# Kernel optimization log

Hardware: AMD Instinct MI355X
Metric: run time of the kernel (lower is better)

The kernel has to match this reference:

```python
import jax, jax.numpy as jnp
import numpy as np

V, N, D, R, L, KS = 32000, 2048, 1024, 16, 4, 7
B, H = 2, 4 * 1024
GMIN, GMAX, ACAP = 0.85, 1.0, 1.0


def rmsnorm(x, w, eps=1e-6):
    return x * jax.lax.rsqrt(jnp.mean(x * x, axis=-1, keepdims=True) + eps) * w


def l2norm(x, eps=1e-8):
    return x / jnp.maximum(jnp.linalg.norm(x, axis=-1, keepdims=True), eps)


def mlp(x, w1, b1, w2, b2):
    return jax.nn.gelu(x @ w1 + b1) @ w2 + b2


def k1_block(h, nw, w1, b1, w2, b2):
    return h + mlp(rmsnorm(h, nw), w1, b1, w2, b2)


def causal_conv(h, kernel):
    # depthwise causal conv with shared 1D kernel; kernel[0] = current step
    n = h.shape[1]
    hp = jnp.pad(h, ((0, 0), (KS - 1, 0), (0, 0)))
    out = jnp.zeros_like(h)
    for k in range(KS):  # KS is small & static
        out = out + kernel[k] * hp[:, KS - 1 - k: KS - 1 - k + n, :]
    return out


def k2_layer(h, p):
    (u, v, dlog, alog, glog, kern, pw, pb, n1w, n2w, w1, b1, w2, b2) = p
    residual = h
    hn = rmsnorm(h, n1w)
    gate = jax.nn.sigmoid(glog)
    out = gate * causal_conv(hn, kern)
    # low-rank q/k
    q = l2norm(hn @ u)          # (B,N,R)
    k = l2norm(hn @ v)          # (B,N,R)
    gamma = GMIN + (GMAX - GMIN) * jax.nn.sigmoid(dlog)   # (R,)
    alpha = ACAP * jax.nn.sigmoid(alog)                   # (R,)
    qa = q * alpha
    pos = jnp.arange(h.shape[1])
    diff = jnp.maximum(pos[:, None] - pos[None, :], 0).astype(h.dtype)
    mask = (pos[:, None] >= pos[None, :]).astype(h.dtype)
    # per-rank causal decay matrix gamma_r^(i-j): (R,N,N)
    decay = jnp.exp(diff[None] * jnp.log(gamma)[:, None, None]) * mask[None]
    scores = jnp.einsum('bir,rij,bjr->bij', qa, decay, k)  # (B,N,N)
    out = out + jnp.einsum('bij,bjd->bid', scores, hn)
    out = out @ pw + pb
    h = residual + out
    h = h + mlp(rmsnorm(h, n2w), w1, b1, w2, b2)
    return h


def setup_inputs() -> dict:
    key = jax.random.key(0)
    ks = jax.random.split(key, 32)
    f32 = jnp.float32
    inp = {
        'tokens': jax.random.randint(ks[0], (B, N), 0, V),
        'emb_table': jax.random.normal(ks[1], (V, D), f32) * 0.02,
        'k1a_nw': jnp.ones((D,), f32),
        'k1a_w1': jax.random.normal(ks[2], (D, H), f32) * 0.02,
        'k1a_b1': jnp.zeros((H,), f32),
        'k1a_w2': jax.random.normal(ks[3], (H, D), f32) * 0.02,
        'k1a_b2': jnp.zeros((D,), f32),
        'k2_u': jax.random.normal(ks[4], (L, D, R), f32) * 0.05,
        'k2_v': jax.random.normal(ks[5], (L, D, R), f32) * 0.05,
        'k2_dlog': jax.random.normal(ks[6], (L, R), f32) * 0.5,
        'k2_alog': jnp.zeros((L, R), f32),
        'k2_glog': jnp.zeros((L,), f32),
        'k2_kern': jax.random.normal(ks[7], (L, KS), f32) * 0.1,
        'k2_pw': jax.random.normal(ks[8], (L, D, D), f32) * 0.02,
        'k2_pb': jnp.zeros((L, D), f32),
        'k2_n1w': jnp.ones((L, D), f32),
        'k2_n2w': jnp.ones((L, D), f32),
        'k2_w1': jax.random.normal(ks[9], (L, D, H), f32) * 0.02,
        'k2_b1': jnp.zeros((L, H), f32),
        'k2_w2': jax.random.normal(ks[10], (L, H, D), f32) * 0.02,
        'k2_b2': jnp.zeros((L, D), f32),
        'k1b_nw': jnp.ones((D,), f32),
        'k1b_w1': jax.random.normal(ks[11], (D, H), f32) * 0.02,
        'k1b_b1': jnp.zeros((H,), f32),
        'k1b_w2': jax.random.normal(ks[12], (H, D), f32) * 0.02,
        'k1b_b2': jnp.zeros((D,), f32),
        'k0_nw': jnp.ones((D,), f32),
        'head_w': jax.random.normal(ks[13], (D, V), f32) * 0.02,
        'head_b': jnp.zeros((V,), f32),
    }
    return inp


def reference(tokens, emb_table,
              k1a_nw, k1a_w1, k1a_b1, k1a_w2, k1a_b2,
              k2_u, k2_v, k2_dlog, k2_alog, k2_glog, k2_kern,
              k2_pw, k2_pb, k2_n1w, k2_n2w, k2_w1, k2_b1, k2_w2, k2_b2,
              k1b_nw, k1b_w1, k1b_b1, k1b_w2, k1b_b2,
              k0_nw, head_w, head_b):
    h = emb_table[tokens]                                  # (B,N,D)
    h = k1_block(h, k1a_nw, k1a_w1, k1a_b1, k1a_w2, k1a_b2)
    stacked = (k2_u, k2_v, k2_dlog, k2_alog, k2_glog, k2_kern,
               k2_pw, k2_pb, k2_n1w, k2_n2w, k2_w1, k2_b1, k2_w2, k2_b2)
    def step(c, p):
        return k2_layer(c, p), None
    h, _ = jax.lax.scan(step, h, stacked)
    h = k1_block(h, k1b_nw, k1b_w1, k1b_b1, k1b_w2, k1b_b2)
    h = rmsnorm(h, k0_nw)                                  # K0 final norm
    return h @ head_w + head_b                             # (B,N,V)
```

## Files before the change

kernel.cpp:

```cpp
#include <hip/hip_runtime.h>
#include <hip/hip_bf16.h>

#define SEQ 2048
#define DIM 1024
#define RNK 16
#define NL 4
#define KT 7
#define BATCH 2
#define HID 4096
#define VOC 32000
#define BNROWS (BATCH*SEQ)
#define CHK 128
#define NCH (SEQ/CHK)
#define PRMS 128
#define KAPP 160

typedef __hip_bfloat16 bf16;
typedef __attribute__((ext_vector_type(8))) short bh8;
typedef __attribute__((ext_vector_type(4))) float vf4;

__device__ __forceinline__ float bfu(unsigned int u) { u <<= 16; return __builtin_bit_cast(float, u); }
__device__ __forceinline__ unsigned short f2bu(float x) { bf16 t = __float2bfloat16(x); return __builtin_bit_cast(unsigned short, t); }
__device__ __forceinline__ float b2f(bf16 x) { return __bfloat162float(x); }
__device__ __forceinline__ float sigm(float x) { return 1.f / (1.f + expf(-x)); }
__device__ __forceinline__ float gelu_t(float x) {
    float u = 0.7978845608028654f * (x + 0.044715f * x * x * x);
    return 0.5f * x * (1.f + tanhf(u));
}

__device__ __forceinline__ void gld16(const bf16* g, bf16* l) {
    __builtin_amdgcn_global_load_lds(
        (const __attribute__((address_space(1))) void*)g,
        (__attribute__((address_space(3))) void*)l,
        16, 0, 0);
}

__global__ void embed_kernel(const int* __restrict__ tokens, const float* __restrict__ emb,
                             float* __restrict__ h) {
    int row = blockIdx.x;
    int tok = tokens[row];
    const float4* src = (const float4*)(emb + (size_t)tok * DIM);
    float4* dst = (float4*)(h + (size_t)row * DIM);
    dst[threadIdx.x] = src[threadIdx.x];
}

__global__ void rmsnorm_kernel(const float* __restrict__ in, const float* __restrict__ wt,
                               bf16* __restrict__ out) {
    int row = blockIdx.x;
    int tx = threadIdx.x;
    float4 v = ((const float4*)(in + (size_t)row * DIM))[tx];
    float ss = v.x * v.x + v.y * v.y + v.z * v.z + v.w * v.w;
#pragma unroll
    for (int off = 32; off > 0; off >>= 1) ss += __shfl_down(ss, off);
    __shared__ float red[4];
    int lane = tx & 63, wv = tx >> 6;
    if (lane == 0) red[wv] = ss;
    __syncthreads();
    float tot = red[0] + red[1] + red[2] + red[3];
    float scale = rsqrtf(tot * (1.f / DIM) + 1e-6f);
    float4 w4 = ((const float4*)wt)[tx];
    uint2 o;
    o.x = f2bu(v.x * scale * w4.x) | ((unsigned int)f2bu(v.y * scale * w4.y) << 16);
    o.y = f2bu(v.z * scale * w4.z) | ((unsigned int)f2bu(v.w * scale * w4.w) << 16);
    *(uint2*)(out + (size_t)row * DIM + tx * 4) = o;
}

__global__ void transpose_cast_kernel(const float* __restrict__ in, bf16* __restrict__ out,
                                      int K, int Nc) {
    __shared__ float tile[32][33];
    int n0 = blockIdx.x * 32, k0 = blockIdx.y * 32;
    int tx = threadIdx.x & 31, ty = threadIdx.x >> 5;
#pragma unroll
    for (int i = 0; i < 32; i += 8)
        tile[ty + i][tx] = in[(size_t)(k0 + ty + i) * Nc + n0 + tx];
    __syncthreads();
#pragma unroll
    for (int i = 0; i < 32; i += 8)
        out[(size_t)(n0 + ty + i) * K + k0 + tx] = __float2bfloat16(tile[tx][ty + i]);
}

__global__ void prep_kernel(const float* __restrict__ dlog, const float* __restrict__ alog,
                            const float* __restrict__ glog, const float* __restrict__ kern,
                            float* __restrict__ prm) {
    int l = blockIdx.x, t = threadIdx.x;
    float* p = prm + l * PRMS;
    if (t < RNK) {
        float g = 0.85f + 0.15f * sigm(dlog[l * RNK + t]);
        float lg = logf(g);
        p[t] = g;
        p[16 + t] = lg;
        p[32 + t] = expf(lg * (float)CHK);
        p[48 + t] = sigm(alog[l * RNK + t]);
    }
    if (t < KT) {
        float gate = sigm(glog[l]);
        p[64 + t] = gate * kern[l * KT + t];
    }
}

__global__ void prep_uv_kernel(const float* __restrict__ u, const float* __restrict__ v,
                               bf16* __restrict__ uvT) {
    int l = blockIdx.y;
    int k = blockIdx.x * 256 + threadIdx.x;
    const float* ul = u + (size_t)l * DIM * RNK;
    const float* vl = v + (size_t)l * DIM * RNK;
    bf16* o = uvT + (size_t)l * 32 * DIM;
#pragma unroll
    for (int r = 0; r < RNK; ++r) {
        o[(size_t)r * DIM + k] = __float2bfloat16(ul[(size_t)k * RNK + r]);
        o[(size_t)(RNK + r) * DIM + k] = __float2bfloat16(vl[(size_t)k * RNK + r]);
    }
}

__global__ void conv_kernel(const bf16* __restrict__ hn, const float* __restrict__ prm,
                            float* __restrict__ Z) {
    int t = blockIdx.x * 256 + threadIdx.x;
    int d4 = (t & 255) * 4;
    int row = t >> 8;
    int n = row & (SEQ - 1);
    float a0 = 0, a1 = 0, a2 = 0, a3 = 0;
#pragma unroll
    for (int kk = 0; kk < KT; ++kk) {
        if (n - kk < 0) break;
        float wv = prm[64 + kk];
        uint2 hv = *(const uint2*)(hn + (size_t)(row - kk) * DIM + d4);
        a0 += wv * bfu(hv.x & 0xffffu);
        a1 += wv * bfu(hv.x >> 16);
        a2 += wv * bfu(hv.y & 0xffffu);
        a3 += wv * bfu(hv.y >> 16);
    }
    float4 o = {a0, a1, a2, a3};
    *(float4*)(Z + (size_t)row * DIM + d4) = o;
}

__global__ __launch_bounds__(64)
void qk_mfma_kernel(const bf16* __restrict__ hn, const bf16* __restrict__ uvT,
                    const float* __restrict__ prm, float* __restrict__ qa,
                    float* __restrict__ kn) {
    int row0 = blockIdx.x * 32;
    int lane = threadIdx.x;
    int fr = lane & 15, kf = (lane >> 4) * 8;
    vf4 acc[2][2] = {};
#pragma unroll 4
    for (int kt = 0; kt < DIM / 32; ++kt) {
        int k0 = kt * 32;
        bh8 b0 = *(const bh8*)(uvT + (size_t)fr * DIM + k0 + kf);
        bh8 b1 = *(const bh8*)(uvT + (size_t)(16 + fr) * DIM + k0 + kf);
        bh8 a0 = *(const bh8*)(hn + (size_t)(row0 + fr) * DIM + k0 + kf);
        bh8 a1 = *(const bh8*)(hn + (size_t)(row0 + 16 + fr) * DIM + k0 + kf);
        acc[0][0] = __builtin_amdgcn_mfma_f32_16x16x32_bf16(a0, b0, acc[0][0], 0, 0, 0);
        acc[0][1] = __builtin_amdgcn_mfma_f32_16x16x32_bf16(a0, b1, acc[0][1], 0, 0, 0);
        acc[1][0] = __builtin_amdgcn_mfma_f32_16x16x32_bf16(a1, b0, acc[1][0], 0, 0, 0);
        acc[1][1] = __builtin_amdgcn_mfma_f32_16x16x32_bf16(a1, b1, acc[1][1], 0, 0, 0);
    }
    int fq = lane >> 4;
    float alpha = prm[48 + fr];
#pragma unroll
    for (int m = 0; m < 2; ++m) {
#pragma unroll
        for (int j = 0; j < 4; ++j) {
            float qv = acc[m][0][j], kv = acc[m][1][j];
            float sq = qv * qv, sk = kv * kv;
#pragma unroll
            for (int mask = 1; mask < 16; mask <<= 1) {
                sq += __shfl_xor(sq, mask);
                sk += __shfl_xor(sk, mask);
            }
            int row = row0 + m * 16 + fq * 4 + j;
            qa[(size_t)row * RNK + fr] = qv / fmaxf(sqrtf(sq), 1e-8f) * alpha;
            kn[(size_t)row * RNK + fr] = kv / fmaxf(sqrtf(sk), 1e-8f);
        }
    }
}

__global__ void trans_hn_kernel(const bf16* __restrict__ hn, bf16* __restrict__ HB) {
    __shared__ bf16 tile[32][40];
    int bc = blockIdx.x;
    int d0 = blockIdx.y * 32, j0 = blockIdx.z * 32;
    int tx = threadIdx.x & 31, ty = threadIdx.x >> 5;
    size_t rowb = (size_t)bc * CHK;
#pragma unroll
    for (int i = 0; i < 32; i += 8)
        tile[ty + i][tx] = hn[(rowb + j0 + ty + i) * DIM + d0 + tx];
    __syncthreads();
    bf16* Hp = HB + (size_t)bc * DIM * KAPP;
#pragma unroll
    for (int i = 0; i < 32; i += 8)
        Hp[(size_t)(d0 + ty + i) * KAPP + j0 + tx] = tile[tx][ty + i];
}

__global__ void scores_kernel(const float* __restrict__ qa, const float* __restrict__ kn,
                              const float* __restrict__ prm, bf16* __restrict__ SA,
                              bf16* __restrict__ kdtB) {
    int bc = blockIdx.x;
    __shared__ float ptab[CHK][16];
    for (int e = threadIdx.x; e < CHK * 16; e += 256) {
        int tt = e >> 4, r = e & 15;
        ptab[tt][r] = expf(prm[16 + r] * (float)tt);
    }
    __syncthreads();
    size_t rowb = (size_t)bc * CHK;
    bf16* SAp = SA + (size_t)bc * CHK * KAPP;
    for (int e = threadIdx.x; e < CHK * CHK; e += 256) {
        int i = e >> 7, j = e & (CHK - 1);
        float vsum = 0.f;
        if (i >= j) {
            const float* qp = qa + (rowb + i) * RNK;
            const float* kp = kn + (rowb + j) * RNK;
#pragma unroll
            for (int r = 0; r < 16; ++r) vsum += qp[r] * ptab[i - j][r] * kp[r];
        }
        SAp[(size_t)i * KAPP + j] = __float2bfloat16(vsum);
    }
    for (int e = threadIdx.x; e < CHK * 32; e += 256) {
        int i = e >> 5, rr = e & 31;
        float w = 0.f;
        if (rr < 16) w = qa[(rowb + i) * RNK + rr] * expf(prm[16 + rr] * (float)(i + 1));
        SAp[(size_t)i * KAPP + CHK + rr] = __float2bfloat16(w);
    }
    bf16* kp2 = kdtB + (size_t)bc * RNK * CHK;
    for (int e = threadIdx.x; e < RNK * CHK; e += 256) {
        int r = e >> 7, j = e & (CHK - 1);
        kp2[e] = __float2bfloat16(ptab[CHK - 1 - j][r] * kn[(rowb + j) * RNK + r]);
    }
}

__global__ __launch_bounds__(64)
void chunkU_kernel(const bf16* __restrict__ HB, const bf16* __restrict__ kdtB,
                   float* __restrict__ U) {
    int bc = blockIdx.x;
    int d0 = blockIdx.y * 64;
    int lane = threadIdx.x;
    int fr = lane & 15, kf = (lane >> 4) * 8;
    const bf16* Hp = HB + (size_t)bc * DIM * KAPP;
    const bf16* Kp = kdtB + (size_t)bc * RNK * CHK;
    vf4 acc[4] = {};
#pragma unroll
    for (int kt = 0; kt < 4; ++kt) {
        int k0 = kt * 32;
        bh8 bb = *(const bh8*)(Kp + (size_t)fr * CHK + k0 + kf);
#pragma unroll
        for (int m = 0; m < 4; ++m) {
            bh8 a = *(const bh8*)(Hp + (size_t)(d0 + m * 16 + fr) * KAPP + k0 + kf);
            acc[m] = __builtin_amdgcn_mfma_f32_16x16x32_bf16(a, bb, acc[m], 0, 0, 0);
        }
    }
    int fq = lane >> 4;
    float* Up = U + (size_t)bc * DIM * RNK;
#pragma unroll
    for (int m = 0; m < 4; ++m)
#pragma unroll
        for (int j = 0; j < 4; ++j)
            Up[(size_t)(d0 + m * 16 + fq * 4 + j) * RNK + fr] = acc[m][j];
}

__global__ void scanP_kernel(const float* __restrict__ U, const float* __restrict__ prm,
                             bf16* __restrict__ HB) {
    int g = blockIdx.x * 256 + threadIdx.x;
    int d = g & (DIM - 1);
    int b = g >> 10;
    float gC[16], p[16];
#pragma unroll
    for (int r = 0; r < 16; ++r) { gC[r] = prm[32 + r]; p[r] = 0.f; }
    for (int c = 0; c < NCH; ++c) {
        int bc = b * NCH + c;
        unsigned int pk[8];
#pragma unroll
        for (int q = 0; q < 8; ++q)
            pk[q] = (unsigned int)f2bu(p[2 * q]) | ((unsigned int)f2bu(p[2 * q + 1]) << 16);
        uint4* dst = (uint4*)(HB + (size_t)bc * DIM * KAPP + (size_t)d * KAPP + CHK);
        dst[0] = make_uint4(pk[0], pk[1], pk[2], pk[3]);
        dst[1] = make_uint4(pk[4], pk[5], pk[6], pk[7]);
        const float4* up = (const float4*)(U + ((size_t)bc * DIM + d) * RNK);
#pragma unroll
        for (int q = 0; q < 4; ++q) {
            float4 u4 = up[q];
            p[4 * q + 0] = gC[4 * q + 0] * p[4 * q + 0] + u4.x;
            p[4 * q + 1] = gC[4 * q + 1] * p[4 * q + 1] + u4.y;
            p[4 * q + 2] = gC[4 * q + 2] * p[4 * q + 2] + u4.z;
            p[4 * q + 3] = gC[4 * q + 3] * p[4 * q + 3] + u4.w;
        }
    }
}

__global__ __launch_bounds__(256)
void apply_gemm_kernel(const bf16* __restrict__ SA, const bf16* __restrict__ HB,
                       const float* __restrict__ Z, bf16* __restrict__ Zb) {
    __shared__ alignas(16) bf16 As[128][40];
    __shared__ alignas(16) bf16 Bs[128][40];
    int bc = blockIdx.y;
    int colB0 = blockIdx.x * 128;
    int t = threadIdx.x;
    int lane = t & 63, wid = t >> 6;
    int wr = wid >> 1, wc = wid & 1;
    vf4 acc[4][4] = {};
    const bf16* A = SA + (size_t)bc * CHK * KAPP;
    const bf16* BT = HB + (size_t)bc * DIM * KAPP;
    int r1 = t >> 2, ko1 = (t & 3) * 8;
    int fr = lane & 15, kf = (lane >> 4) * 8;
#pragma unroll
    for (int kt = 0; kt < 5; ++kt) {
        int k0 = kt * 32;
        int4 va1 = *(const int4*)(A + (size_t)r1 * KAPP + k0 + ko1);
        int4 va2 = *(const int4*)(A + (size_t)(r1 + 64) * KAPP + k0 + ko1);
        int4 vb1 = *(const int4*)(BT + (size_t)(colB0 + r1) * KAPP + k0 + ko1);
        int4 vb2 = *(const int4*)(BT + (size_t)(colB0 + r1 + 64) * KAPP + k0 + ko1);
        __syncthreads();
        *(int4*)&As[r1][ko1] = va1;
        *(int4*)&As[r1 + 64][ko1] = va2;
        *(int4*)&Bs[r1][ko1] = vb1;
        *(int4*)&Bs[r1 + 64][ko1] = vb2;
        __syncthreads();
        bh8 a[4], bb[4];
#pragma unroll
        for (int m = 0; m < 4; ++m) a[m] = *(const bh8*)&As[wr * 64 + m * 16 + fr][kf];
#pragma unroll
        for (int n = 0; n < 4; ++n) bb[n] = *(const bh8*)&Bs[wc * 64 + n * 16 + fr][kf];
#pragma unroll
        for (int m = 0; m < 4; ++m)
#pragma unroll
            for (int n = 0; n < 4; ++n)
                acc[m][n] = __builtin_amdgcn_mfma_f32_16x16x32_bf16(a[m], bb[n], acc[m][n], 0, 0, 0);
    }
    int fq = lane >> 4;
    size_t rowb = (size_t)bc * CHK;
#pragma unroll
    for (int m = 0; m < 4; ++m) {
#pragma unroll
        for (int n = 0; n < 4; ++n) {
            int col = colB0 + wc * 64 + n * 16 + fr;
#pragma unroll
            for (int j = 0; j < 4; ++j) {
                size_t row = rowb + wr * 64 + m * 16 + fq * 4 + j;
                size_t idx = row * DIM + col;
                Zb[idx] = __float2bfloat16(Z[idx] + acc[m][n][j]);
            }
        }
    }
}

template <int EPI>
__global__ __launch_bounds__(256)
void gemm_kernel(const bf16* __restrict__ A, const bf16* __restrict__ BT,
                 const float* __restrict__ bias, const float* __restrict__ res,
                 float* __restrict__ outF, bf16* __restrict__ outB,
                 int M, int Nc, int K, int lda) {
    __shared__ alignas(16) bf16 As[128][32];
    __shared__ alignas(16) bf16 Bs[128][32];
    int gx = gridDim.x;
    int orig = blockIdx.y * gx + blockIdx.x;
    int qch = (gx * gridDim.y) >> 3;
    int wg = (orig & 7) * qch + (orig >> 3);
    int bn = wg % gx, bm = wg / gx;
    int t = threadIdx.x;
    int lane = t & 63, wid = t >> 6;
    int wr = wid >> 1, wc = wid & 1;
    vf4 acc[4][4] = {};
    const int rowA0 = bm * 128, colB0 = bn * 128;
    int fr = lane & 15, kf = (lane >> 4) * 8;
    int c0 = wid * 2;
    int lrow = lane >> 2;
    int lcol = (lane & 3) * 8;
    const bf16* Ag0 = A + (size_t)(rowA0 + c0 * 16 + lrow) * lda + lcol;
    const bf16* Ag1 = A + (size_t)(rowA0 + c0 * 16 + 16 + lrow) * lda + lcol;
    const bf16* Bg0 = BT + (size_t)(colB0 + c0 * 16 + lrow) * lda + lcol;
    const bf16* Bg1 = BT + (size_t)(colB0 + c0 * 16 + 16 + lrow) * lda + lcol;
    bf16* Al0 = &As[0][0] + c0 * 512;
    bf16* Al1 = Al0 + 512;
    bf16* Bl0 = &Bs[0][0] + c0 * 512;
    bf16* Bl1 = Bl0 + 512;
    int nk = K >> 5;
    for (int kt = 0; kt < nk; ++kt) {
        int k0 = kt * 32;
        __syncthreads();
        gld16(Ag0 + k0, Al0);
        gld16(Ag1 + k0, Al1);
        gld16(Bg0 + k0, Bl0);
        gld16(Bg1 + k0, Bl1);
        asm volatile("s_waitcnt vmcnt(0)" ::: "memory");
        __syncthreads();
        bh8 a[4], bb[4];
#pragma unroll
        for (int m = 0; m < 4; ++m) a[m] = *(const bh8*)&As[wr * 64 + m * 16 + fr][kf];
#pragma unroll
        for (int n = 0; n < 4; ++n) bb[n] = *(const bh8*)&Bs[wc * 64 + n * 16 + fr][kf];
#pragma unroll
        for (int m = 0; m < 4; ++m)
#pragma unroll
            for (int n = 0; n < 4; ++n)
                acc[m][n] = __builtin_amdgcn_mfma_f32_16x16x32_bf16(a[m], bb[n], acc[m][n], 0, 0, 0);
    }
    int fq = lane >> 4;
#pragma unroll
    for (int m = 0; m < 4; ++m) {
#pragma unroll
        for (int n = 0; n < 4; ++n) {
            int col = colB0 + wc * 64 + n * 16 + fr;
            float bv = bias[col];
#pragma unroll
            for (int j = 0; j < 4; ++j) {
                int row = rowA0 + wr * 64 + m * 16 + fq * 4 + j;
                size_t idx = (size_t)row * Nc + col;
                float v2 = acc[m][n][j] + bv;
                if (EPI == 1) v2 += res[idx];
                outF[idx] = v2;
            }
        }
    }
}

#define SB __builtin_amdgcn_sched_barrier(0)
template <int EPI>
__global__ __launch_bounds__(512, 2)
void gemm256_kernel(const bf16* __restrict__ A, const bf16* __restrict__ BT,
                    const float* __restrict__ bias,
                    float* __restrict__ outF, bf16* __restrict__ outB,
                    int M, int Nc, int K, int lda) {
    extern __shared__ char smem[];
    bf16* Alds = (bf16*)smem;
    bf16* Blds = (bf16*)(smem + 65536);
    if (EPI == 3) {
        size_t zo = (size_t)blockIdx.z * K;
        A += zo; BT += zo;
        outF += (size_t)blockIdx.z * ((size_t)M * Nc);
    }
    int gx = gridDim.x, gy = gridDim.y;
    int orig = blockIdx.y * gx + blockIdx.x;
    int qch = (gx * gy) >> 3;
    int wg = (orig & 7) * qch + (orig >> 3);
    int bm = wg % gy, bn = wg / gy;
    int rowA0 = bm * 256, colB0 = bn * 256;
    int tid = threadIdx.x;
    int lane = tid & 63, wid = tid >> 6;
    int wm = wid >> 2, wn = wid & 3;
    int fr = lane & 15;
    int kf8 = ((((lane >> 4) & 3) ^ ((fr >> 1) & 3)) * 8);
    int srow = wid * 16 + (lane >> 2);
    int scol = (((lane & 3) ^ ((lane >> 3) & 3)) * 8);
    const bf16* Ags = A + (size_t)(rowA0 + srow) * lda + scol;
    const bf16* Bgs = BT + (size_t)(colB0 + srow) * lda + scol;
    int sbase = wid * 512;
    auto stA = [&](int d, int kh, int k0) {
        bf16* dst = Alds + (d * 2 + kh) * 8192 + sbase;
        const bf16* src = Ags + k0 + kh * 32;
        gld16(src, dst);
        gld16(src + (size_t)128 * lda, dst + 4096);
    };
    auto stB = [&](int d, int kh, int k0) {
        bf16* dst = Blds + (d * 2 + kh) * 8192 + sbase;
        const bf16* src = Bgs + k0 + kh * 32;
        gld16(src, dst);
        gld16(src + (size_t)128 * lda, dst + 4096);
    };
    const bf16* Ard = Alds + (size_t)(wm * 128 + fr) * 32 + kf8;
    const bf16* Brd = Blds + (size_t)(wn * 64 + fr) * 32 + kf8;
    vf4 acc[8][4] = {};
    int nt = K >> 6;
    stA(0, 0, 0); stB(0, 0, 0); stA(0, 1, 0); stB(0, 1, 0);
    for (int t = 0; t < nt; ++t) {
        int d = t & 1, nd = d ^ 1;
        int k1 = (t + 1) << 6;
        bool pf = (t + 1 < nt);
        int dof = d * 16384;
        bh8 bF[4];
        if (pf) { stA(nd, 0, k1); asm volatile("s_waitcnt vmcnt(6)" ::: "memory"); }
        else    {                 asm volatile("s_waitcnt vmcnt(4)" ::: "memory"); }
        SB; __builtin_amdgcn_s_barrier(); SB;
        {
            bh8 a0 = *(const bh8*)(Ard + dof + 0 * 512);
            bh8 a1 = *(const bh8*)(Ard + dof + 1 * 512);
            bh8 a2 = *(const bh8*)(Ard + dof + 2 * 512);
            bh8 a3 = *(const bh8*)(Ard + dof + 3 * 512);
#pragma unroll
            for (int n = 0; n < 4; ++n) bF[n] = *(const bh8*)(Brd + dof + n * 512);
            __builtin_amdgcn_s_setprio(1);
#pragma unroll
            for (int n = 0; n < 4; ++n) {
                acc[0][n] = __builtin_amdgcn_mfma_f32_16x16x32_bf16(a0, bF[n], acc[0][n], 0, 0, 0);
                acc[1][n] = __builtin_amdgcn_mfma_f32_16x16x32_bf16(a1, bF[n], acc[1][n], 0, 0, 0);
                acc[2][n] = __builtin_amdgcn_mfma_f32_16x16x32_bf16(a2, bF[n], acc[2][n], 0, 0, 0);
                acc[3][n] = __builtin_amdgcn_mfma_f32_16x16x32_bf16(a3, bF[n], acc[3][n], 0, 0, 0);
            }
            __builtin_amdgcn_s_setprio(0);
        }
        SB;
        if (pf) stB(nd, 0, k1);
        SB; __builtin_amdgcn_s_barrier(); SB;
        {
            bh8 a0 = *(const bh8*)(Ard + dof + 4 * 512);
            bh8 a1 = *(const bh8*)(Ard + dof + 5 * 512);
            bh8 a2 = *(const bh8*)(Ard + dof + 6 * 512);
            bh8 a3 = *(const bh8*)(Ard + dof + 7 * 512);
            __builtin_amdgcn_s_setprio(1);
#pragma unroll
            for (int n = 0; n < 4; ++n) {
                acc[4][n] = __builtin_amdgcn_mfma_f32_16x16x32_bf16(a0, bF[n], acc[4][n], 0, 0, 0);
                acc[5][n] = __builtin_amdgcn_mfma_f32_16x16x32_bf16(a1, bF[n], acc[5][n], 0, 0, 0);
                acc[6][n] = __builtin_amdgcn_mfma_f32_16x16x32_bf16(a2, bF[n], acc[6][n], 0, 0, 0);
                acc[7][n] = __builtin_amdgcn_mfma_f32_16x16x32_bf16(a3, bF[n], acc[7][n], 0, 0, 0);
            }
            __builtin_amdgcn_s_setprio(0);
        }
        SB;
        int dof1 = dof + 8192;
        if (pf) { stA(nd, 1, k1); asm volatile("s_waitcnt vmcnt(6)" ::: "memory"); }
        else    {                 asm volatile("s_waitcnt vmcnt(0)" ::: "memory"); }
        SB; __builtin_amdgcn_s_barrier(); SB;
        {
            bh8 a0 = *(const bh8*)(Ard + dof1 + 0 * 512);
            bh8 a1 = *(const bh8*)(Ard + dof1 + 1 * 512);
            bh8 a2 = *(const bh8*)(Ard + dof1 + 2 * 512);
            bh8 a3 = *(const bh8*)(Ard + dof1 + 3 * 512);
#pragma unroll
            for (int n = 0; n < 4; ++n) bF[n] = *(const bh8*)(Brd + dof1 + n * 512);
            __builtin_amdgcn_s_setprio(1);
#pragma unroll
            for (int n = 0; n < 4; ++n) {
                acc[0][n] = __builtin_amdgcn_mfma_f32_16x16x32_bf16(a0, bF[n], acc[0][n], 0, 0, 0);
                acc[1][n] = __builtin_amdgcn_mfma_f32_16x16x32_bf16(a1, bF[n], acc[1][n], 0, 0, 0);
                acc[2][n] = __builtin_amdgcn_mfma_f32_16x16x32_bf16(a2, bF[n], acc[2][n], 0, 0, 0);
                acc[3][n] = __builtin_amdgcn_mfma_f32_16x16x32_bf16(a3, bF[n], acc[3][n], 0, 0, 0);
            }
            __builtin_amdgcn_s_setprio(0);
        }
        SB;
        if (pf) stB(nd, 1, k1);
        SB; __builtin_amdgcn_s_barrier(); SB;
        {
            bh8 a0 = *(const bh8*)(Ard + dof1 + 4 * 512);
            bh8 a1 = *(const bh8*)(Ard + dof1 + 5 * 512);
            bh8 a2 = *(const bh8*)(Ard + dof1 + 6 * 512);
            bh8 a3 = *(const bh8*)(Ard + dof1 + 7 * 512);
            __builtin_amdgcn_s_setprio(1);
#pragma unroll
            for (int n = 0; n < 4; ++n) {
                acc[4][n] = __builtin_amdgcn_mfma_f32_16x16x32_bf16(a0, bF[n], acc[4][n], 0, 0, 0);
                acc[5][n] = __builtin_amdgcn_mfma_f32_16x16x32_bf16(a1, bF[n], acc[5][n], 0, 0, 0);
                acc[6][n] = __builtin_amdgcn_mfma_f32_16x16x32_bf16(a2, bF[n], acc[6][n], 0, 0, 0);
                acc[7][n] = __builtin_amdgcn_mfma_f32_16x16x32_bf16(a3, bF[n], acc[7][n], 0, 0, 0);
            }
            __builtin_amdgcn_s_setprio(0);
        }
        SB;
    }
    int fq = lane >> 4;
#pragma unroll
    for (int mi = 0; mi < 8; ++mi) {
#pragma unroll
        for (int ni = 0; ni < 4; ++ni) {
            int col = colB0 + wn * 64 + ni * 16 + fr;
            float bv = (EPI == 3) ? 0.f : bias[col];
#pragma unroll
            for (int j = 0; j < 4; ++j) {
                int row = rowA0 + wm * 128 + mi * 16 + fq * 4 + j;
                size_t idx = (size_t)row * Nc + col;
                float v2 = acc[mi][ni][j] + bv;
                if (EPI == 2) outB[idx] = __float2bfloat16(gelu_t(v2));
                else outF[idx] = v2;
            }
        }
    }
}

__global__ void combine4_norm_kernel(const float* __restrict__ P, const float* __restrict__ bias,
                                     const float* __restrict__ nw, float* __restrict__ h,
                                     bf16* __restrict__ hnb) {
    int row = blockIdx.x;
    int tx = threadIdx.x;
    int t = row * 256 + tx;
    const size_t S = (size_t)BNROWS * DIM;
    float4 p0 = ((const float4*)P)[t];
    float4 p1 = ((const float4*)(P + S))[t];
    float4 p2 = ((const float4*)(P + 2 * S))[t];
    float4 p3 = ((const float4*)(P + 3 * S))[t];
    float4 bv = ((const float4*)bias)[tx];
    float4 hv = ((float4*)h)[t];
    hv.x += (p0.x + p1.x) + (p2.x + p3.x) + bv.x;
    hv.y += (p0.y + p1.y) + (p2.y + p3.y) + bv.y;
    hv.z += (p0.z + p1.z) + (p2.z + p3.z) + bv.z;
    hv.w += (p0.w + p1.w) + (p2.w + p3.w) + bv.w;
    ((float4*)h)[t] = hv;
    float ss = hv.x * hv.x + hv.y * hv.y + hv.z * hv.z + hv.w * hv.w;
#pragma unroll
    for (int off = 32; off > 0; off >>= 1) ss += __shfl_down(ss, off);
    __shared__ float red[4];
    int lane = tx & 63, wv = tx >> 6;
    if (lane == 0) red[wv] = ss;
    __syncthreads();
    float tot = red[0] + red[1] + red[2] + red[3];
    float scale = rsqrtf(tot * (1.f / DIM) + 1e-6f);
    float4 w4 = ((const float4*)nw)[tx];
    uint2 o;
    o.x = f2bu(hv.x * scale * w4.x) | ((unsigned int)f2bu(hv.y * scale * w4.y) << 16);
    o.y = f2bu(hv.z * scale * w4.z) | ((unsigned int)f2bu(hv.w * scale * w4.w) << 16);
    *(uint2*)(hnb + (size_t)row * DIM + tx * 4) = o;
}

extern "C" void kernel_launch(void* const* d_in, const int* in_sizes, int n_in,
                              void* d_out, int out_size, void* d_ws, size_t ws_size,
                              hipStream_t stream) {
    (void)in_sizes; (void)n_in; (void)out_size; (void)ws_size;
    const int* tokens = (const int*)d_in[0];
    const float* emb = (const float*)d_in[1];
    const float* k1a_nw = (const float*)d_in[2];
    const float* k1a_w1 = (const float*)d_in[3];
    const float* k1a_b1 = (const float*)d_in[4];
    const float* k1a_w2 = (const float*)d_in[5];
    const float* k1a_b2 = (const float*)d_in[6];
    const float* k2_u = (const float*)d_in[7];
    const float* k2_v = (const float*)d_in[8];
    const float* k2_dlog = (const float*)d_in[9];
    const float* k2_alog = (const float*)d_in[10];
    const float* k2_glog = (const float*)d_in[11];
    const float* k2_kern = (const float*)d_in[12];
    const float* k2_pw = (const float*)d_in[13];
    const float* k2_pb = (const float*)d_in[14];
    const float* k2_n1w = (const float*)d_in[15];
    const float* k2_n2w = (const float*)d_in[16];
    const float* k2_w1 = (const float*)d_in[17];
    const float* k2_b1 = (const float*)d_in[18];
    const float* k2_w2 = (const float*)d_in[19];
    const float* k2_b2 = (const float*)d_in[20];
    const float* k1b_nw = (const float*)d_in[21];
    const float* k1b_w1 = (const float*)d_in[22];
    const float* k1b_b1 = (const float*)d_in[23];
    const float* k1b_w2 = (const float*)d_in[24];
    const float* k1b_b2 = (const float*)d_in[25];
    const float* k0_nw = (const float*)d_in[26];
    const float* head_w = (const float*)d_in[27];
    const float* head_b = (const float*)d_in[28];
    float* out = (float*)d_out;

    (void)hipFuncSetAttribute((const void*)gemm256_kernel<0>,
                              hipFuncAttributeMaxDynamicSharedMemorySize, 131072);
    (void)hipFuncSetAttribute((const void*)gemm256_kernel<2>,
                              hipFuncAttributeMaxDynamicSharedMemorySize, 131072);
    (void)hipFuncSetAttribute((const void*)gemm256_kernel<3>,
                              hipFuncAttributeMaxDynamicSharedMemorySize, 131072);

    char* wsp = (char*)d_ws;
    auto alloc = [&](size_t bytes) -> char* {
        char* p = wsp;
        wsp += (bytes + 255) & ~(size_t)255;
        return p;
    };
    float* h   = (float*)alloc((size_t)BNROWS * DIM * 4);
    float* Z   = (float*)alloc((size_t)BNROWS * DIM * 4);
    bf16* hnb  = (bf16*)alloc((size_t)BNROWS * DIM * 2);
    bf16* Zb   = (bf16*)alloc((size_t)BNROWS * DIM * 2);
    bf16* t1b  = (bf16*)alloc((size_t)BNROWS * HID * 2);
    float* qaB = (float*)alloc((size_t)BNROWS * RNK * 4);
    float* knB = (float*)alloc((size_t)BNROWS * RNK * 4);
    float* U   = (float*)alloc((size_t)BATCH * NCH * DIM * RNK * 4);
    bf16* HB   = (bf16*)alloc((size_t)BATCH * NCH * DIM * KAPP * 2);
    bf16* SA   = (bf16*)alloc((size_t)BATCH * NCH * CHK * KAPP * 2);
    bf16* kdtB = (bf16*)alloc((size_t)BATCH * NCH * RNK * CHK * 2);
    float* prm = (float*)alloc((size_t)NL * PRMS * 4);
    bf16* uvT  = (bf16*)alloc((size_t)NL * 32 * DIM * 2);
    bf16* w1aT = (bf16*)alloc((size_t)HID * DIM * 2);
    bf16* w2aT = (bf16*)alloc((size_t)DIM * HID * 2);
    bf16* w1bT = (bf16*)alloc((size_t)HID * DIM * 2);
    bf16* w2bT = (bf16*)alloc((size_t)DIM * HID * 2);
    bf16* pwT  = (bf16*)alloc((size_t)NL * DIM * DIM * 2);
    bf16* w1T  = (bf16*)alloc((size_t)NL * DIM * HID * 2);
    bf16* w2T  = (bf16*)alloc((size_t)NL * HID * DIM * 2);
    bf16* headT = (bf16*)alloc((size_t)VOC * DIM * 2);
    float* Pk  = (float*)alloc((size_t)4 * BNROWS * DIM * 4);

    hipMemsetAsync(HB, 0, (size_t)BATCH * NCH * DIM * KAPP * 2, stream);

    auto T = [&](const float* in, bf16* o, int K, int Nc) {
        transpose_cast_kernel<<<dim3(Nc / 32, K / 32), 256, 0, stream>>>(in, o, K, Nc);
    };
    T(k1a_w1, w1aT, DIM, HID);
    T(k1a_w2, w2aT, HID, DIM);
    T(k1b_w1, w1bT, DIM, HID);
    T(k1b_w2, w2bT, HID, DIM);
    for (int l = 0; l < NL; ++l) {
        T(k2_pw + (size_t)l * DIM * DIM, pwT + (size_t)l * DIM * DIM, DIM, DIM);
        T(k2_w1 + (size_t)l * DIM * HID, w1T + (size_t)l * DIM * HID, DIM, HID);
        T(k2_w2 + (size_t)l * HID * DIM, w2T + (size_t)l * HID * DIM, HID, DIM);
    }
    T(head_w, headT, DIM, VOC);
    prep_kernel<<<NL, 32, 0, stream>>>(k2_dlog, k2_alog, k2_glog, k2_kern, prm);
    prep_uv_kernel<<<dim3(DIM / 256, NL), 256, 0, stream>>>(k2_u, k2_v, uvT);

    auto mlp_core = [&](const bf16* W1, const float* B1, const bf16* W2, const float* B2,
                        const float* nw_next) {
        gemm256_kernel<2><<<dim3(HID / 256, BNROWS / 256), 512, 131072, stream>>>(
            hnb, W1, B1, nullptr, t1b, BNROWS, HID, DIM, DIM);
        gemm256_kernel<3><<<dim3(DIM / 256, BNROWS / 256, 4), 512, 131072, stream>>>(
            t1b, W2, nullptr, Pk, nullptr, BNROWS, DIM, HID / 4, HID);
        combine4_norm_kernel<<<BNROWS, 256, 0, stream>>>(Pk, B2, nw_next, h, hnb);
    };

    embed_kernel<<<BNROWS, 256, 0, stream>>>(tokens, emb, h);
    rmsnorm_kernel<<<BNROWS, 256, 0, stream>>>(h, k1a_nw, hnb);
    mlp_core(w1aT, k1a_b1, w2aT, k1a_b2, k2_n1w);

    for (int l = 0; l < NL; ++l) {
        const float* prm_l = prm + l * PRMS;
        conv_kernel<<<BNROWS, 256, 0, stream>>>(hnb, prm_l, Z);
        qk_mfma_kernel<<<BNROWS / 32, 64, 0, stream>>>(hnb, uvT + (size_t)l * 32 * DIM,
                                                       prm_l, qaB, knB);
        trans_hn_kernel<<<dim3(BATCH * NCH, DIM / 32, CHK / 32), 256, 0, stream>>>(hnb, HB);
        scores_kernel<<<BATCH * NCH, 256, 0, stream>>>(qaB, knB, prm_l, SA, kdtB);
        chunkU_kernel<<<dim3(BATCH * NCH, DIM / 64), 64, 0, stream>>>(HB, kdtB, U);
        scanP_kernel<<<BATCH * DIM / 256, 256, 0, stream>>>(U, prm_l, HB);
        apply_gemm_kernel<<<dim3(DIM / 128, BATCH * NCH), 256, 0, stream>>>(SA, HB, Z, Zb);
        gemm_kernel<1><<<dim3(DIM / 128, BNROWS / 128), 256, 0, stream>>>(
            Zb, pwT + (size_t)l * DIM * DIM, k2_pb + (size_t)l * DIM, h, h, nullptr,
            BNROWS, DIM, DIM, DIM);
        rmsnorm_kernel<<<BNROWS, 256, 0, stream>>>(h, k2_n2w + (size_t)l * DIM, hnb);
        const float* nw_next = (l < NL - 1) ? (k2_n1w + (size_t)(l + 1) * DIM) : k1b_nw;
        mlp_core(w1T + (size_t)l * DIM * HID, k2_b1 + (size_t)l * HID,
                 w2T + (size_t)l * HID * DIM, k2_b2 + (size_t)l * DIM, nw_next);
    }

    mlp_core(w1bT, k1b_b1, w2bT, k1b_b2, k0_nw);

    gemm256_kernel<0><<<dim3(VOC / 256, BNROWS / 256), 512, 131072, stream>>>(
        hnb, headT, head_b, out, nullptr, BNROWS, VOC, DIM, DIM);
}
```

Measured before the change: 1.711 ms.

## Reschedule GEMM main loop to issue LDS reads before barriers and prefetch

Restructures the 256-tile GEMM inner loop so each phase's LDS fragment reads are issued before the global-to-LDS prefetch and the workgroup barrier, with an explicit lgkmcnt wait just before the MFMAs. Global-load vmcnt waits and the initial prologue barrier are reorganized, and an extra barrier is added at the end of each iteration. The aim is to overlap LDS read latency with barrier wait and global prefetch issue. In exchange, each iteration has one more barrier, and the reordered vmcnt counts carry a risk of subtle LDS read/write hazards.

```diff
diff --git a/kernel.cpp b/kernel.cpp
--- a/kernel.cpp
+++ b/kernel.cpp
@@ -410,6 +410,7 @@
 }
 
 #define SB __builtin_amdgcn_sched_barrier(0)
+#define LGKM0 do { asm volatile("s_waitcnt lgkmcnt(0)" ::: "memory"); SB; } while (0)
 template <int EPI>
 __global__ __launch_bounds__(512, 2)
 void gemm256_kernel(const bf16* __restrict__ A, const bf16* __restrict__ BT,
@@ -457,91 +458,89 @@
     vf4 acc[8][4] = {};
     int nt = K >> 6;
     stA(0, 0, 0); stB(0, 0, 0); stA(0, 1, 0); stB(0, 1, 0);
+    asm volatile("s_waitcnt vmcnt(4)" ::: "memory");
+    SB; __builtin_amdgcn_s_barrier(); SB;
     for (int t = 0; t < nt; ++t) {
         int d = t & 1, nd = d ^ 1;
         int k1 = (t + 1) << 6;
         bool pf = (t + 1 < nt);
         int dof = d * 16384;
-        bh8 bF[4];
-        if (pf) { stA(nd, 0, k1); asm volatile("s_waitcnt vmcnt(6)" ::: "memory"); }
-        else    {                 asm volatile("s_waitcnt vmcnt(4)" ::: "memory"); }
-        SB; __builtin_amdgcn_s_barrier(); SB;
-        {
-            bh8 a0 = *(const bh8*)(Ard + dof + 0 * 512);
-            bh8 a1 = *(const bh8*)(Ard + dof + 1 * 512);
-            bh8 a2 = *(const bh8*)(Ard + dof + 2 * 512);
-            bh8 a3 = *(const bh8*)(Ard + dof + 3 * 512);
-#pragma unroll
-            for (int n = 0; n < 4; ++n) bF[n] = *(const bh8*)(Brd + dof + n * 512);
-            __builtin_amdgcn_s_setprio(1);
-#pragma unroll
-            for (int n = 0; n < 4; ++n) {
-                acc[0][n] = __builtin_amdgcn_mfma_f32_16x16x32_bf16(a0, bF[n], acc[0][n], 0, 0, 0);
-                acc[1][n] = __builtin_amdgcn_mfma_f32_16x16x32_bf16(a1, bF[n], acc[1][n], 0, 0, 0);
-                acc[2][n] = __builtin_amdgcn_mfma_f32_16x16x32_bf16(a2, bF[n], acc[2][n], 0, 0, 0);
-                acc[3][n] = __builtin_amdgcn_mfma_f32_16x16x32_bf16(a3, bF[n], acc[3][n], 0, 0, 0);
-            }
-            __builtin_amdgcn_s_setprio(0);
-        }
+        int dof1 = dof + 8192;
+        bh8 a0, a1, a2, a3, bF[4];
+        a0 = *(const bh8*)(Ard + dof + 0 * 512);
+        a1 = *(const bh8*)(Ard + dof + 1 * 512);
+        a2 = *(const bh8*)(Ard + dof + 2 * 512);
+        a3 = *(const bh8*)(Ard + dof + 3 * 512);
+#pragma unroll
+        for (int n = 0; n < 4; ++n) bF[n] = *(const bh8*)(Brd + dof + n * 512);
         SB;
-        if (pf) stB(nd, 0, k1);
-        SB; __builtin_amdgcn_s_barrier(); SB;
-        {
-            bh8 a0 = *(const bh8*)(Ard + dof + 4 * 512);
-            bh8 a1 = *(const bh8*)(Ard + dof + 5 * 512);
-            bh8 a2 = *(const bh8*)(Ard + dof + 6 * 512);
-            bh8 a3 = *(const bh8*)(Ard + dof + 7 * 512);
-            __builtin_amdgcn_s_setprio(1);
-#pragma unroll
-            for (int n = 0; n < 4; ++n) {
-                acc[4][n] = __builtin_amdgcn_mfma_f32_16x16x32_bf16(a0, bF[n], acc[4][n], 0, 0, 0);
-                acc[5][n] = __builtin_amdgcn_mfma_f32_16x16x32_bf16(a1, bF[n], acc[5][n], 0, 0, 0);
-                acc[6][n] = __builtin_amdgcn_mfma_f32_16x16x32_bf16(a2, bF[n], acc[6][n], 0, 0, 0);
-                acc[7][n] = __builtin_amdgcn_mfma_f32_16x16x32_bf16(a3, bF[n], acc[7][n], 0, 0, 0);
-            }
-            __builtin_amdgcn_s_setprio(0);
-        }
+        if (pf) stA(nd, 0, k1);
+        SB; __builtin_amdgcn_s_barrier(); LGKM0;
+        __builtin_amdgcn_s_setprio(1);
+#pragma unroll
+        for (int n = 0; n < 4; ++n) {
+            acc[0][n] = __builtin_amdgcn_mfma_f32_16x16x32_bf16(a0, bF[n], acc[0][n], 0, 0, 0);
+            acc[1][n] = __builtin_amdgcn_mfma_f32_16x16x32_bf16(a1, bF[n], acc[1][n], 0, 0, 0);
+            acc[2][n] = __builtin_amdgcn_mfma_f32_16x16x32_bf16(a2, bF[n], acc[2][n], 0, 0, 0);
+            acc[3][n] = __builtin_amdgcn_mfma_f32_16x16x32_bf16(a3, bF[n], acc[3][n], 0, 0, 0);
+        }
+        __builtin_amdgcn_s_setprio(0);
         SB;
-        int dof1 = dof + 8192;
-        if (pf) { stA(nd, 1, k1); asm volatile("s_waitcnt vmcnt(6)" ::: "memory"); }
+        a0 = *(const bh8*)(Ard + dof + 4 * 512);
+        a1 = *(const bh8*)(Ard + dof + 5 * 512);
+        a2 = *(const bh8*)(Ard + dof + 6 * 512);
+        a3 = *(const bh8*)(Ard + dof + 7 * 512);
+        SB;
+        if (pf) { stB(nd, 0, k1); asm volatile("s_waitcnt vmcnt(4)" ::: "memory"); }
         else    {                 asm volatile("s_waitcnt vmcnt(0)" ::: "memory"); }
-        SB; __builtin_amdgcn_s_barrier(); SB;
-        {
-            bh8 a0 = *(const bh8*)(Ard + dof1 + 0 * 512);
-            bh8 a1 = *(const bh8*)(Ard + dof1 + 1 * 512);
-            bh8 a2 = *(const bh8*)(Ard + dof1 + 2 * 512);
-            bh8 a3 = *(const bh8*)(Ard + dof1 + 3 * 512);
-#pragma unroll
-            for (int n = 0; n < 4; ++n) bF[n] = *(const bh8*)(Brd + dof1 + n * 512);
-            __builtin_amdgcn_s_setprio(1);
-#pragma unroll
-            for (int n = 0; n < 4; ++n) {
-                acc[0][n] = __builtin_amdgcn_mfma_f32_16x16x32_bf16(a0, bF[n], acc[0][n], 0, 0, 0);
-                acc[1][n] = __builtin_amdgcn_mfma_f32_16x16x32_bf16(a1, bF[n], acc[1][n], 0, 0, 0);
-                acc[2][n] = __builtin_amdgcn_mfma_f32_16x16x32_bf16(a2, bF[n], acc[2][n], 0, 0, 0);
-                acc[3][n] = __builtin_amdgcn_mfma_f32_16x16x32_bf16(a3, bF[n], acc[3][n], 0, 0, 0);
-            }
-            __builtin_amdgcn_s_setprio(0);
-        }
+        SB; __builtin_amdgcn_s_barrier(); LGKM0;
+        __builtin_amdgcn_s_setprio(1);
+#pragma unroll
+        for (int n = 0; n < 4; ++n) {
+            acc[4][n] = __builtin_amdgcn_mfma_f32_16x16x32_bf16(a0, bF[n], acc[4][n], 0, 0, 0);
+            acc[5][n] = __builtin_amdgcn_mfma_f32_16x16x32_bf16(a1, bF[n], acc[5][n], 0, 0, 0);
+            acc[6][n] = __builtin_amdgcn_mfma_f32_16x16x32_bf16(a2, bF[n], acc[6][n], 0, 0, 0);
+            acc[7][n] = __builtin_amdgcn_mfma_f32_16x16x32_bf16(a3, bF[n], acc[7][n], 0, 0, 0);
+        }
+        __builtin_amdgcn_s_setprio(0);
         SB;
-        if (pf) stB(nd, 1, k1);
-        SB; __builtin_amdgcn_s_barrier(); SB;
-        {
-            bh8 a0 = *(const bh8*)(Ard + dof1 + 4 * 512);
-            bh8 a1 = *(const bh8*)(Ard + dof1 + 5 * 512);
-            bh8 a2 = *(const bh8*)(Ard + dof1 + 6 * 512);
-            bh8 a3 = *(const bh8*)(Ard + dof1 + 7 * 512);
-            __builtin_amdgcn_s_setprio(1);
-#pragma unroll
-            for (int n = 0; n < 4; ++n) {
-                acc[4][n] = __builtin_amdgcn_mfma_f32_16x16x32_bf16(a0, bF[n], acc[4][n], 0, 0, 0);
-                acc[5][n] = __builtin_amdgcn_mfma_f32_16x16x32_bf16(a1, bF[n], acc[5][n], 0, 0, 0);
-                acc[6][n] = __builtin_amdgcn_mfma_f32_16x16x32_bf16(a2, bF[n], acc[6][n], 0, 0, 0);
-                acc[7][n] = __builtin_amdgcn_mfma_f32_16x16x32_bf16(a3, bF[n], acc[7][n], 0, 0, 0);
-            }
-            __builtin_amdgcn_s_setprio(0);
-        }
+        a0 = *(const bh8*)(Ard + dof1 + 0 * 512);
+        a1 = *(const bh8*)(Ard + dof1 + 1 * 512);
+        a2 = *(const bh8*)(Ard + dof1 + 2 * 512);
+        a3 = *(const bh8*)(Ard + dof1 + 3 * 512);
+#pragma unroll
+        for (int n = 0; n < 4; ++n) bF[n] = *(const bh8*)(Brd + dof1 + n * 512);
         SB;
+        if (pf) stA(nd, 1, k1);
+        SB; __builtin_amdgcn_s_barrier(); LGKM0;
+        __builtin_amdgcn_s_setprio(1);
+#pragma unroll
+        for (int n = 0; n < 4; ++n) {
+            acc[0][n] = __builtin_amdgcn_mfma_f32_16x16x32_bf16(a0, bF[n], acc[0][n], 0, 0, 0);
+            acc[1][n] = __builtin_amdgcn_mfma_f32_16x16x32_bf16(a1, bF[n], acc[1][n], 0, 0, 0);
+            acc[2][n] = __builtin_amdgcn_mfma_f32_16x16x32_bf16(a2, bF[n], acc[2][n], 0, 0, 0);
+            acc[3][n] = __builtin_amdgcn_mfma_f32_16x16x32_bf16(a3, bF[n], acc[3][n], 0, 0, 0);
+        }
+        __builtin_amdgcn_s_setprio(0);
+        SB;
+        a0 = *(const bh8*)(Ard + dof1 + 4 * 512);
+        a1 = *(const bh8*)(Ard + dof1 + 5 * 512);
+        a2 = *(const bh8*)(Ard + dof1 + 6 * 512);
+        a3 = *(const bh8*)(Ard + dof1 + 7 * 512);
+        SB;
+        if (pf) { stB(nd, 1, k1); asm volatile("s_waitcnt vmcnt(4)" ::: "memory"); }
+        SB; __builtin_amdgcn_s_barrier(); LGKM0;
+        __builtin_amdgcn_s_setprio(1);
+#pragma unroll
+        for (int n = 0; n < 4; ++n) {
+            acc[4][n] = __builtin_amdgcn_mfma_f32_16x16x32_bf16(a0, bF[n], acc[4][n], 0, 0, 0);
+            acc[5][n] = __builtin_amdgcn_mfma_f32_16x16x32_bf16(a1, bF[n], acc[5][n], 0, 0, 0);
+            acc[6][n] = __builtin_amdgcn_mfma_f32_16x16x32_bf16(a2, bF[n], acc[6][n], 0, 0, 0);
+            acc[7][n] = __builtin_amdgcn_mfma_f32_16x16x32_bf16(a3, bF[n], acc[7][n], 0, 0, 0);
+        }
+        __builtin_amdgcn_s_setprio(0);
+        SB;
+        __builtin_amdgcn_s_barrier(); SB;
     }
     int fq = lane >> 4;
 #pragma unroll
```

Measured after the change: 1.729 ms. No clear change (+1.1%).
